# Performance work log

Measured on AMD Instinct MI355X. Metric: run time of the kernel, lower is better.

The kernel has to match this reference:

```python
import jax, jax.numpy as jnp
import numpy as np

# Mamba hyperparams derived from DRMamba.__init__: d_model=dim=96, d_state=16, d_conv=4, expand=2
D_MODEL = 96
D_INNER = 192          # expand * d_model
D_STATE = 16
D_CONV = 4
DT_RANK = 6            # ceil(d_model / 16)
REVERSE = True


def setup_inputs() -> dict:
    key = jax.random.key(0)
    ks = jax.random.split(key, 8)
    s = lambda k, shape: jax.random.normal(k, shape, jnp.float32) * 0.02
    x = jax.random.normal(ks[0], (8, 96, 64, 64), jnp.float32)
    in_proj_w = s(ks[1], (2 * D_INNER, D_MODEL))
    conv_w = s(ks[2], (D_INNER, 1, D_CONV))            # depthwise conv kernel (O, I/groups=1, K)
    conv_b = jnp.zeros((D_INNER,), jnp.float32)
    x_proj_w = s(ks[3], (DT_RANK + 2 * D_STATE, D_INNER))
    dt_proj_w = s(ks[4], (D_INNER, DT_RANK))
    dt_proj_b = s(ks[5], (D_INNER,))
    # S4D-real init, as in standard Mamba
    A_log = jnp.log(jnp.broadcast_to(jnp.arange(1, D_STATE + 1, dtype=jnp.float32), (D_INNER, D_STATE)))
    D = jnp.ones((D_INNER,), jnp.float32)
    out_proj_w = s(ks[6], (D_MODEL, D_INNER))
    return dict(x=x, in_proj_w=in_proj_w, conv_w=conv_w, conv_b=conv_b,
                x_proj_w=x_proj_w, dt_proj_w=dt_proj_w, dt_proj_b=dt_proj_b,
                A_log=A_log, D=D, out_proj_w=out_proj_w)


def reference(x, in_proj_w, conv_w, conv_b, x_proj_w, dt_proj_w, dt_proj_b, A_log, D, out_proj_w):
    b, c, h, w = x.shape
    xs = jnp.flip(x, 1) if REVERSE else x
    seq = xs.reshape(b, c, h * w).transpose(0, 2, 1)              # (b, l, d_model)
    xz = seq @ in_proj_w.T                                        # (b, l, 2*d_inner)
    u, res = jnp.split(xz, 2, axis=-1)
    # causal depthwise conv1d over sequence (torch: padding=d_conv-1 then truncate to l)
    uc = jax.lax.conv_general_dilated(
        u.transpose(0, 2, 1), conv_w, (1,), [(D_CONV - 1, 0)],
        dimension_numbers=('NCH', 'OIH', 'NCH'), feature_group_count=D_INNER)
    uc = uc + conv_b[None, :, None]
    u = jax.nn.silu(uc.transpose(0, 2, 1))                        # (b, l, d_inner)
    # input-dependent SSM parameters
    dbc = u @ x_proj_w.T                                          # (b, l, dt_rank + 2*d_state)
    dt, B, C = jnp.split(dbc, [DT_RANK, DT_RANK + D_STATE], axis=-1)
    delta = jax.nn.softplus(dt @ dt_proj_w.T + dt_proj_b)         # (b, l, d_inner)
    A = -jnp.exp(A_log)                                           # (d_inner, d_state)
    dA = jnp.exp(jnp.einsum('bld,dn->bldn', delta, A))            # discretized A
    dBu = jnp.einsum('bld,bln,bld->bldn', delta, B, u)            # discretized B * u

    def step(state, inp):
        dA_t, dBu_t, C_t = inp                                    # (b,d,n), (b,d,n), (b,n)
        state = dA_t * state + dBu_t
        y_t = jnp.einsum('bdn,bn->bd', state, C_t)
        return state, y_t

    init = jnp.zeros((b, D_INNER, D_STATE), u.dtype)
    _, ys = jax.lax.scan(step, init,
                         (dA.transpose(1, 0, 2, 3), dBu.transpose(1, 0, 2, 3), C.transpose(1, 0, 2)))
    y = ys.transpose(1, 0, 2) + u * D                             # (b, l, d_inner)
    y = y * jax.nn.silu(res)
    out = y @ out_proj_w.T                                        # (b, l, d_model)
    out = out.transpose(0, 2, 1).reshape(b, c, h, w)
    return jnp.flip(out, 1) if REVERSE else out
```

## Files before the change

kernel.cpp:

```cpp
#include <hip/hip_runtime.h>
#include <math.h>

#define NBATCH 8
#define SEQL   4096
#define DMODEL 96
#define DINNER 192
#define DSTATE 16
#define NDBC   38
#define NCHUNK 128
#define CSTEP  32

__device__ __forceinline__ float siluf(float x) {
    return x / (1.f + expf(-x));
}
__device__ __forceinline__ float silu_fast(float x) {
    return x * __builtin_amdgcn_rcpf(1.f + __expf(-x));
}
__device__ __forceinline__ float softplus_fast(float x) {
    return (x > 15.f) ? x : __logf(1.f + __expf(x));
}

__global__ __launch_bounds__(256) void k_in_proj(const float* __restrict__ x,
                                                 const float* __restrict__ w,
                                                 float* __restrict__ u_raw,
                                                 float* __restrict__ res)
{
    __shared__ float As[32][128];
    __shared__ float Wt[32][133];
    const int tid = threadIdx.x;
    const int jg = tid & 15;
    const int lg = tid >> 4;
    const int b = blockIdx.z;
    const int l0 = blockIdx.x * 128;
    const int jb = blockIdx.y * 128;

    float acc[8][8];
#pragma unroll
    for (int r = 0; r < 8; r++)
#pragma unroll
        for (int c = 0; c < 8; c++) acc[r][c] = 0.f;

    for (int kb = 0; kb < 3; kb++) {
        {
            const int ll4 = tid & 31;
            const int m0 = tid >> 5;
#pragma unroll
            for (int i = 0; i < 4; i++) {
                const int m = m0 + 8 * i;
                const float4 v = *reinterpret_cast<const float4*>(
                    &x[((size_t)b * 96 + (95 - (kb * 32 + m))) * 4096 + l0 + ll4 * 4]);
                *reinterpret_cast<float4*>(&As[m][ll4 * 4]) = v;
            }
        }
        {
            const int k4 = tid & 7;
            const int jl0 = tid >> 3;
#pragma unroll
            for (int i = 0; i < 4; i++) {
                const int jl = jl0 + 32 * i;
                const float4 v = *reinterpret_cast<const float4*>(
                    &w[(size_t)(jb + jl) * 96 + kb * 32 + k4 * 4]);
                Wt[k4 * 4 + 0][jl] = v.x;
                Wt[k4 * 4 + 1][jl] = v.y;
                Wt[k4 * 4 + 2][jl] = v.z;
                Wt[k4 * 4 + 3][jl] = v.w;
            }
        }
        __syncthreads();
#pragma unroll
        for (int k = 0; k < 32; k++) {
            const float4 a0 = *reinterpret_cast<const float4*>(&As[k][lg * 8]);
            const float4 a1 = *reinterpret_cast<const float4*>(&As[k][lg * 8 + 4]);
            const float4 w0 = *reinterpret_cast<const float4*>(&Wt[k][jg * 8]);
            const float4 w1 = *reinterpret_cast<const float4*>(&Wt[k][jg * 8 + 4]);
            const float av[8] = {a0.x, a0.y, a0.z, a0.w, a1.x, a1.y, a1.z, a1.w};
            const float wv[8] = {w0.x, w0.y, w0.z, w0.w, w1.x, w1.y, w1.z, w1.w};
#pragma unroll
            for (int r = 0; r < 8; r++)
#pragma unroll
                for (int c = 0; c < 8; c++) acc[r][c] = fmaf(av[r], wv[c], acc[r][c]);
        }
        __syncthreads();
    }

    const int j0 = jb + jg * 8;
    float* outp;
    int col0;
    if (j0 < 192) { outp = u_raw; col0 = j0; }
    else          { outp = res;   col0 = j0 - 192; }
#pragma unroll
    for (int r = 0; r < 8; r++) {
        const int row = l0 + lg * 8 + r;
        float* rowp = &outp[((size_t)b * 4096 + row) * 192 + col0];
        *reinterpret_cast<float4*>(rowp) =
            make_float4(acc[r][0], acc[r][1], acc[r][2], acc[r][3]);
        *reinterpret_cast<float4*>(rowp + 4) =
            make_float4(acc[r][4], acc[r][5], acc[r][6], acc[r][7]);
    }
}

__global__ __launch_bounds__(256) void k_xproj(const float* __restrict__ u_raw,
                                               const float* __restrict__ w,
                                               const float* __restrict__ cw,
                                               const float* __restrict__ cb,
                                               float* __restrict__ dtarr,
                                               float* __restrict__ Barr,
                                               float* __restrict__ Carr)
{
    __shared__ float Ur[67][33];
    __shared__ float Us[64][36];
    __shared__ float Ws[64 * 32];
    const int tid = threadIdx.x, tx = tid & 15, ty = tid >> 4;
    const int b = blockIdx.y;
    const int l0 = blockIdx.x * 64;

    float acc[4][4];
#pragma unroll
    for (int r = 0; r < 4; r++)
#pragma unroll
        for (int c = 0; c < 4; c++) acc[r][c] = 0.f;

    const int ch = tid & 31;
    const int lblk = tid >> 5;

    for (int kb = 0; kb < 6; kb++) {
        for (int idx = tid; idx < 536; idx += 256) {
            const int row = idx >> 3;
            const int c4 = idx & 7;
            const int gl = l0 - 3 + row;
            float4 v = make_float4(0.f, 0.f, 0.f, 0.f);
            if (gl >= 0)
                v = *reinterpret_cast<const float4*>(
                    &u_raw[((size_t)b * 4096 + gl) * 192 + kb * 32 + c4 * 4]);
            Ur[row][c4 * 4 + 0] = v.x;
            Ur[row][c4 * 4 + 1] = v.y;
            Ur[row][c4 * 4 + 2] = v.z;
            Ur[row][c4 * 4 + 3] = v.w;
        }
        {
            const int k4 = tid & 7;
            const int jb0 = tid >> 3;
#pragma unroll
            for (int i = 0; i < 2; i++) {
                const int jl = jb0 + 32 * i;
                float4 v = make_float4(0.f, 0.f, 0.f, 0.f);
                if (jl < NDBC)
                    v = *reinterpret_cast<const float4*>(&w[(size_t)jl * 192 + kb * 32 + k4 * 4]);
                *reinterpret_cast<float4*>(
                    &Ws[jl * 32 + ((k4 ^ ((jl >> 2) & 7)) << 2)]) = v;
            }
        }
        __syncthreads();

        {
            const float4 wc = *reinterpret_cast<const float4*>(&cw[(kb * 32 + ch) * 4]);
            const float bias = cb[kb * 32 + ch];
#pragma unroll
            for (int r = 0; r < 8; r++) {
                const int l = lblk * 8 + r;
                float s = bias;
                s = fmaf(wc.x, Ur[l + 0][ch], s);
                s = fmaf(wc.y, Ur[l + 1][ch], s);
                s = fmaf(wc.z, Ur[l + 2][ch], s);
                s = fmaf(wc.w, Ur[l + 3][ch], s);
                Us[l][ch] = siluf(s);
            }
        }
        __syncthreads();

        const int sw = tx & 7;
#pragma unroll
        for (int k4 = 0; k4 < 8; k4++) {
            float4 a4[4];
#pragma unroll
            for (int r = 0; r < 4; r++)
                a4[r] = *reinterpret_cast<const float4*>(&Us[ty * 4 + r][k4 * 4]);
            float4 w4[4];
#pragma unroll
            for (int c = 0; c < 4; c++)
                w4[c] = *reinterpret_cast<const float4*>(
                    &Ws[(tx * 4 + c) * 32 + ((k4 ^ sw) << 2)]);
#pragma unroll
            for (int r = 0; r < 4; r++)
#pragma unroll
                for (int c = 0; c < 4; c++) {
                    acc[r][c] = fmaf(a4[r].x, w4[c].x, acc[r][c]);
                    acc[r][c] = fmaf(a4[r].y, w4[c].y, acc[r][c]);
                    acc[r][c] = fmaf(a4[r].z, w4[c].z, acc[r][c]);
                    acc[r][c] = fmaf(a4[r].w, w4[c].w, acc[r][c]);
                }
        }
        __syncthreads();
    }

#pragma unroll
    for (int r = 0; r < 4; r++) {
        const size_t row = (size_t)b * 4096 + l0 + ty * 4 + r;
#pragma unroll
        for (int c = 0; c < 4; c++) {
            const int j = tx * 4 + c;
            if (j < 6)       dtarr[row * 8 + j] = acc[r][c];
            else if (j < 22) Barr[row * 16 + (j - 6)] = acc[r][c];
            else if (j < 38) Carr[row * 16 + (j - 22)] = acc[r][c];
        }
    }
}

__global__ __launch_bounds__(192) void k_scan1(const float* __restrict__ u_raw,
                                               const float* __restrict__ dtarr,
                                               const float* __restrict__ Barr,
                                               const float* __restrict__ A_log,
                                               const float* __restrict__ dt_w,
                                               const float* __restrict__ dt_b,
                                               const float* __restrict__ cw,
                                               const float* __restrict__ cb,
                                               float* __restrict__ P,
                                               float* __restrict__ S)
{
    const int d = threadIdx.x;
    const int c = blockIdx.x;
    const int b = blockIdx.y;

    float a[16];
    {
        const float4* al = reinterpret_cast<const float4*>(&A_log[d * 16]);
#pragma unroll
        for (int i = 0; i < 4; i++) {
            const float4 v = al[i];
            a[4 * i + 0] = -expf(v.x);
            a[4 * i + 1] = -expf(v.y);
            a[4 * i + 2] = -expf(v.z);
            a[4 * i + 3] = -expf(v.w);
        }
    }
    float dw[6];
#pragma unroll
    for (int k = 0; k < 6; k++) dw[k] = dt_w[d * 6 + k];
    const float db = dt_b[d];
    const float4 wc = *reinterpret_cast<const float4*>(&cw[d * 4]);
    const float cbias = cb[d];

    float st[16], p[16];
#pragma unroll
    for (int n = 0; n < 16; n++) { st[n] = 0.f; p[n] = 1.f; }

    const int t0 = c * CSTEP;
    const size_t g0 = (size_t)b * 4096 + t0;
    const float* up = u_raw + g0 * 192 + d;
    const float* dtp = dtarr + g0 * 8;
    const float* bp = Barr + g0 * 16;

    float w0 = 0.f, w1 = 0.f, w2 = 0.f;
    if (t0 >= 3) {
        w0 = up[-3 * 192];
        w1 = up[-2 * 192];
        w2 = up[-1 * 192];
    }

#pragma unroll 2
    for (int t = 0; t < CSTEP; t++) {
        const float w3 = up[t * 192];
        float uc = cbias;
        uc = fmaf(wc.x, w0, uc);
        uc = fmaf(wc.y, w1, uc);
        uc = fmaf(wc.z, w2, uc);
        uc = fmaf(wc.w, w3, uc);
        w0 = w1; w1 = w2; w2 = w3;
        const float ut = silu_fast(uc);

        const float4 q0 = *reinterpret_cast<const float4*>(dtp + t * 8);
        const float4 q1 = *reinterpret_cast<const float4*>(dtp + t * 8 + 4);
        float s = db;
        s = fmaf(q0.x, dw[0], s); s = fmaf(q0.y, dw[1], s);
        s = fmaf(q0.z, dw[2], s); s = fmaf(q0.w, dw[3], s);
        s = fmaf(q1.x, dw[4], s); s = fmaf(q1.y, dw[5], s);
        const float dt = softplus_fast(s);
        const float dtu = dt * ut;

        float Bv[16];
        {
            const float4* b4 = reinterpret_cast<const float4*>(bp + t * 16);
#pragma unroll
            for (int i = 0; i < 4; i++) {
                const float4 v = b4[i];
                Bv[4 * i + 0] = v.x; Bv[4 * i + 1] = v.y;
                Bv[4 * i + 2] = v.z; Bv[4 * i + 3] = v.w;
            }
        }
#pragma unroll
        for (int n = 0; n < 16; n++) {
            const float dA = __expf(dt * a[n]);
            p[n] *= dA;
            st[n] = fmaf(dA, st[n], dtu * Bv[n]);
        }
    }

    const size_t idx = (((size_t)b * NCHUNK + c) * 192 + d) * 16;
    float4* Pp = reinterpret_cast<float4*>(&P[idx]);
    float4* Sp = reinterpret_cast<float4*>(&S[idx]);
#pragma unroll
    for (int i = 0; i < 4; i++) {
        Pp[i] = make_float4(p[4 * i], p[4 * i + 1], p[4 * i + 2], p[4 * i + 3]);
        Sp[i] = make_float4(st[4 * i], st[4 * i + 1], st[4 * i + 2], st[4 * i + 3]);
    }
}

__global__ __launch_bounds__(256) void k_scan2(const float* __restrict__ P,
                                               float* __restrict__ S)
{
    const int dn = blockIdx.x * 256 + threadIdx.x;
    const int b = blockIdx.y;
    float carry = 0.f;
    const size_t base = (size_t)b * NCHUNK * 3072 + dn;
#pragma unroll 8
    for (int c = 0; c < NCHUNK; c++) {
        const size_t idx = base + (size_t)c * 3072;
        const float p = P[idx];
        const float s = S[idx];
        S[idx] = carry;
        carry = fmaf(p, carry, s);
    }
}

__global__ __launch_bounds__(192) void k_scan3(const float* __restrict__ u_raw,
                                               const float* __restrict__ dtarr,
                                               const float* __restrict__ Barr,
                                               const float* __restrict__ Carr,
                                               const float* __restrict__ A_log,
                                               const float* __restrict__ dt_w,
                                               const float* __restrict__ dt_b,
                                               const float* __restrict__ cw,
                                               const float* __restrict__ cb,
                                               const float* __restrict__ S,
                                               const float* __restrict__ Dp,
                                               const float* __restrict__ res,
                                               float* __restrict__ y)
{
    const int d = threadIdx.x;
    const int c = blockIdx.x;
    const int b = blockIdx.y;

    float a[16];
    {
        const float4* al = reinterpret_cast<const float4*>(&A_log[d * 16]);
#pragma unroll
        for (int i = 0; i < 4; i++) {
            const float4 v = al[i];
            a[4 * i + 0] = -expf(v.x);
            a[4 * i + 1] = -expf(v.y);
            a[4 * i + 2] = -expf(v.z);
            a[4 * i + 3] = -expf(v.w);
        }
    }
    float dw[6];
#pragma unroll
    for (int k = 0; k < 6; k++) dw[k] = dt_w[d * 6 + k];
    const float db = dt_b[d];
    const float4 wc = *reinterpret_cast<const float4*>(&cw[d * 4]);
    const float cbias = cb[d];
    const float Dd = Dp[d];

    float st[16];
    {
        const float4* Sp = reinterpret_cast<const float4*>(
            &S[(((size_t)b * NCHUNK + c) * 192 + d) * 16]);
#pragma unroll
        for (int i = 0; i < 4; i++) {
            const float4 v = Sp[i];
            st[4 * i + 0] = v.x; st[4 * i + 1] = v.y;
            st[4 * i + 2] = v.z; st[4 * i + 3] = v.w;
        }
    }

    const int t0 = c * CSTEP;
    const size_t g0 = (size_t)b * 4096 + t0;
    const float* up = u_raw + g0 * 192 + d;
    const float* rp = res + g0 * 192 + d;
    float* yp = y + g0 * 192 + d;
    const float* dtp = dtarr + g0 * 8;
    const float* bp = Barr + g0 * 16;
    const float* cp = Carr + g0 * 16;

    float w0 = 0.f, w1 = 0.f, w2 = 0.f;
    if (t0 >= 3) {
        w0 = up[-3 * 192];
        w1 = up[-2 * 192];
        w2 = up[-1 * 192];
    }

#pragma unroll 2
    for (int t = 0; t < CSTEP; t++) {
        const float w3 = up[t * 192];
        float uc = cbias;
        uc = fmaf(wc.x, w0, uc);
        uc = fmaf(wc.y, w1, uc);
        uc = fmaf(wc.z, w2, uc);
        uc = fmaf(wc.w, w3, uc);
        w0 = w1; w1 = w2; w2 = w3;
        const float ut = silu_fast(uc);

        const float4 q0 = *reinterpret_cast<const float4*>(dtp + t * 8);
        const float4 q1 = *reinterpret_cast<const float4*>(dtp + t * 8 + 4);
        float s = db;
        s = fmaf(q0.x, dw[0], s); s = fmaf(q0.y, dw[1], s);
        s = fmaf(q0.z, dw[2], s); s = fmaf(q0.w, dw[3], s);
        s = fmaf(q1.x, dw[4], s); s = fmaf(q1.y, dw[5], s);
        const float dt = softplus_fast(s);
        const float dtu = dt * ut;

        float Bv[16], Cv[16];
        {
            const float4* b4 = reinterpret_cast<const float4*>(bp + t * 16);
            const float4* c4 = reinterpret_cast<const float4*>(cp + t * 16);
#pragma unroll
            for (int i = 0; i < 4; i++) {
                const float4 v = b4[i];
                Bv[4 * i + 0] = v.x; Bv[4 * i + 1] = v.y;
                Bv[4 * i + 2] = v.z; Bv[4 * i + 3] = v.w;
                const float4 w = c4[i];
                Cv[4 * i + 0] = w.x; Cv[4 * i + 1] = w.y;
                Cv[4 * i + 2] = w.z; Cv[4 * i + 3] = w.w;
            }
        }
        float yt = 0.f;
#pragma unroll
        for (int n = 0; n < 16; n++) {
            const float dA = __expf(dt * a[n]);
            st[n] = fmaf(dA, st[n], dtu * Bv[n]);
            yt = fmaf(st[n], Cv[n], yt);
        }
        const float r = rp[t * 192];
        yp[t * 192] = fmaf(ut, Dd, yt) * silu_fast(r);
    }
}

__global__ __launch_bounds__(256) void k_outproj(const float* __restrict__ y,
                                                 const float* __restrict__ w,
                                                 float* __restrict__ out)
{
    __shared__ float Ws[64 * 32];
    const int tid = threadIdx.x, tx = tid & 15, ty = tid >> 4;
    const int b = blockIdx.z;
    const int l0 = blockIdx.x * 128;
    const int jb = blockIdx.y * 64;

    float acc[8][4];
#pragma unroll
    for (int r = 0; r < 8; r++)
#pragma unroll
        for (int c = 0; c < 4; c++) acc[r][c] = 0.f;

    for (int kb = 0; kb < 6; kb++) {
        {
            const int k4 = tid & 7;
            const int jb0 = tid >> 3;
#pragma unroll
            for (int i = 0; i < 2; i++) {
                const int jl = jb0 + 32 * i;
                const int j = jb + jl;
                float4 v = make_float4(0.f, 0.f, 0.f, 0.f);
                if (j < 96)
                    v = *reinterpret_cast<const float4*>(&w[(size_t)j * 192 + kb * 32 + k4 * 4]);
                *reinterpret_cast<float4*>(
                    &Ws[jl * 32 + ((k4 ^ ((jl >> 2) & 7)) << 2)]) = v;
            }
        }
        __syncthreads();
        const int sw = tx & 7;
#pragma unroll
        for (int k4 = 0; k4 < 8; k4++) {
            float4 a4[8];
#pragma unroll
            for (int r = 0; r < 8; r++) {
                const int row = l0 + ty * 8 + r;
                a4[r] = *reinterpret_cast<const float4*>(
                    &y[((size_t)b * 4096 + row) * 192 + kb * 32 + k4 * 4]);
            }
            float4 w4[4];
#pragma unroll
            for (int c = 0; c < 4; c++)
                w4[c] = *reinterpret_cast<const float4*>(
                    &Ws[(tx * 4 + c) * 32 + ((k4 ^ sw) << 2)]);
#pragma unroll
            for (int r = 0; r < 8; r++)
#pragma unroll
                for (int c = 0; c < 4; c++) {
                    acc[r][c] = fmaf(a4[r].x, w4[c].x, acc[r][c]);
                    acc[r][c] = fmaf(a4[r].y, w4[c].y, acc[r][c]);
                    acc[r][c] = fmaf(a4[r].z, w4[c].z, acc[r][c]);
                    acc[r][c] = fmaf(a4[r].w, w4[c].w, acc[r][c]);
                }
        }
        __syncthreads();
    }
#pragma unroll
    for (int c = 0; c < 4; c++) {
        const int j = jb + tx * 4 + c;
        if (j < 96) {
            const int ch = 95 - j;
            const float4 v0 = make_float4(acc[0][c], acc[1][c], acc[2][c], acc[3][c]);
            const float4 v1 = make_float4(acc[4][c], acc[5][c], acc[6][c], acc[7][c]);
            const size_t base = ((size_t)b * 96 + ch) * 4096 + l0 + ty * 8;
            *reinterpret_cast<float4*>(&out[base]) = v0;
            *reinterpret_cast<float4*>(&out[base + 4]) = v1;
        }
    }
}

extern "C" void kernel_launch(void* const* d_in, const int* in_sizes, int n_in,
                              void* d_out, int out_size, void* d_ws, size_t ws_size,
                              hipStream_t stream)
{
    const float* x       = (const float*)d_in[0];
    const float* in_w    = (const float*)d_in[1];
    const float* conv_w  = (const float*)d_in[2];
    const float* conv_b  = (const float*)d_in[3];
    const float* xproj_w = (const float*)d_in[4];
    const float* dt_w    = (const float*)d_in[5];
    const float* dt_b    = (const float*)d_in[6];
    const float* A_log   = (const float*)d_in[7];
    const float* Dp      = (const float*)d_in[8];
    const float* out_w   = (const float*)d_in[9];

    float* ws    = (float*)d_ws;
    float* u_raw = ws;
    float* res   = u_raw + 6291456;
    float* yfin  = res   + 6291456;
    float* dtarr = yfin  + 6291456;
    float* Barr  = dtarr + 262144;
    float* Carr  = Barr  + 524288;
    float* P     = Carr  + 524288;
    float* S     = P     + 3145728;

    hipLaunchKernelGGL(k_in_proj, dim3(32, 3, 8), dim3(256), 0, stream, x, in_w, u_raw, res);
    hipLaunchKernelGGL(k_xproj,   dim3(64, 8),    dim3(256), 0, stream,
                       u_raw, xproj_w, conv_w, conv_b, dtarr, Barr, Carr);
    hipLaunchKernelGGL(k_scan1,   dim3(NCHUNK, 8), dim3(192), 0, stream,
                       u_raw, dtarr, Barr, A_log, dt_w, dt_b, conv_w, conv_b, P, S);
    hipLaunchKernelGGL(k_scan2,   dim3(12, 8),    dim3(256), 0, stream, P, S);
    hipLaunchKernelGGL(k_scan3,   dim3(NCHUNK, 8), dim3(192), 0, stream,
                       u_raw, dtarr, Barr, Carr, A_log, dt_w, dt_b, conv_w, conv_b,
                       S, Dp, res, yfin);
    hipLaunchKernelGGL(k_outproj, dim3(32, 2, 8), dim3(256), 0, stream, yfin, out_w, (float*)d_out);
}
```

Measured before the change: 274.0 us.

## Retile in_proj GEMM with 512-thread blocks, 256-row by 64-column tiles

Restructures the input projection GEMM. Each block now covers 256 sequence positions by 64 output columns with 512 threads, and each thread computes 4 rows by 8 columns, where before it was 128x128 tiles, 256 threads and 8x8 per thread. Within a wave, every lane reads its own A values while all lanes read the same W values as a broadcast. The goal is to cut LDS bank conflicts, lower register pressure for better occupancy, and raise the block count. In exchange, each thread does less arithmetic per LDS load, and each block reloads the x tile for every 64-column slice, which increases global reads of x.

```diff
diff --git a/kernel.cpp b/kernel.cpp
--- a/kernel.cpp
+++ b/kernel.cpp
@@ -20,77 +20,70 @@
     return (x > 15.f) ? x : __logf(1.f + __expf(x));
 }
 
-__global__ __launch_bounds__(256) void k_in_proj(const float* __restrict__ x,
+__global__ __launch_bounds__(512) void k_in_proj(const float* __restrict__ x,
                                                  const float* __restrict__ w,
                                                  float* __restrict__ u_raw,
                                                  float* __restrict__ res)
 {
-    __shared__ float As[32][128];
-    __shared__ float Wt[32][133];
+    __shared__ float As[32][256];
+    __shared__ float Wt[32][72];
     const int tid = threadIdx.x;
-    const int jg = tid & 15;
-    const int lg = tid >> 4;
+    const int lane = tid & 63;
+    const int wv = tid >> 6;
     const int b = blockIdx.z;
-    const int l0 = blockIdx.x * 128;
-    const int jb = blockIdx.y * 128;
-
-    float acc[8][8];
-#pragma unroll
-    for (int r = 0; r < 8; r++)
+    const int l0 = blockIdx.y * 256;
+    const int jb = blockIdx.x * 64;
+    const int j0 = jb + wv * 8;
+
+    float acc[4][8];
+#pragma unroll
+    for (int r = 0; r < 4; r++)
 #pragma unroll
         for (int c = 0; c < 8; c++) acc[r][c] = 0.f;
 
     for (int kb = 0; kb < 3; kb++) {
+#pragma unroll
+        for (int i = 0; i < 4; i++) {
+            const int idx = tid + 512 * i;
+            const int m = idx >> 6;
+            const int c4 = idx & 63;
+            const float4 v = *reinterpret_cast<const float4*>(
+                &x[((size_t)b * 96 + (95 - (kb * 32 + m))) * 4096 + l0 + c4 * 4]);
+            *reinterpret_cast<float4*>(&As[m][c4 * 4]) = v;
+        }
         {
-            const int ll4 = tid & 31;
-            const int m0 = tid >> 5;
-#pragma unroll
-            for (int i = 0; i < 4; i++) {
-                const int m = m0 + 8 * i;
-                const float4 v = *reinterpret_cast<const float4*>(
-                    &x[((size_t)b * 96 + (95 - (kb * 32 + m))) * 4096 + l0 + ll4 * 4]);
-                *reinterpret_cast<float4*>(&As[m][ll4 * 4]) = v;
-            }
-        }
-        {
-            const int k4 = tid & 7;
-            const int jl0 = tid >> 3;
-#pragma unroll
-            for (int i = 0; i < 4; i++) {
-                const int jl = jl0 + 32 * i;
-                const float4 v = *reinterpret_cast<const float4*>(
-                    &w[(size_t)(jb + jl) * 96 + kb * 32 + k4 * 4]);
-                Wt[k4 * 4 + 0][jl] = v.x;
-                Wt[k4 * 4 + 1][jl] = v.y;
-                Wt[k4 * 4 + 2][jl] = v.z;
-                Wt[k4 * 4 + 3][jl] = v.w;
-            }
+            const int j = tid & 63;
+            const int k4 = tid >> 6;
+            const float4 v = *reinterpret_cast<const float4*>(
+                &w[(size_t)(jb + j) * 96 + kb * 32 + k4 * 4]);
+            Wt[k4 * 4 + 0][j] = v.x;
+            Wt[k4 * 4 + 1][j] = v.y;
+            Wt[k4 * 4 + 2][j] = v.z;
+            Wt[k4 * 4 + 3][j] = v.w;
         }
         __syncthreads();
 #pragma unroll
         for (int k = 0; k < 32; k++) {
-            const float4 a0 = *reinterpret_cast<const float4*>(&As[k][lg * 8]);
-            const float4 a1 = *reinterpret_cast<const float4*>(&As[k][lg * 8 + 4]);
-            const float4 w0 = *reinterpret_cast<const float4*>(&Wt[k][jg * 8]);
-            const float4 w1 = *reinterpret_cast<const float4*>(&Wt[k][jg * 8 + 4]);
-            const float av[8] = {a0.x, a0.y, a0.z, a0.w, a1.x, a1.y, a1.z, a1.w};
-            const float wv[8] = {w0.x, w0.y, w0.z, w0.w, w1.x, w1.y, w1.z, w1.w};
-#pragma unroll
-            for (int r = 0; r < 8; r++)
-#pragma unroll
-                for (int c = 0; c < 8; c++) acc[r][c] = fmaf(av[r], wv[c], acc[r][c]);
-        }
-        __syncthreads();
-    }
-
-    const int j0 = jb + jg * 8;
+            const float4 a4 = *reinterpret_cast<const float4*>(&As[k][lane * 4]);
+            const float4 wA = *reinterpret_cast<const float4*>(&Wt[k][wv * 8]);
+            const float4 wB = *reinterpret_cast<const float4*>(&Wt[k][wv * 8 + 4]);
+            const float av[4] = {a4.x, a4.y, a4.z, a4.w};
+            const float wvv[8] = {wA.x, wA.y, wA.z, wA.w, wB.x, wB.y, wB.z, wB.w};
+#pragma unroll
+            for (int r = 0; r < 4; r++)
+#pragma unroll
+                for (int c = 0; c < 8; c++) acc[r][c] = fmaf(av[r], wvv[c], acc[r][c]);
+        }
+        __syncthreads();
+    }
+
     float* outp;
     int col0;
     if (j0 < 192) { outp = u_raw; col0 = j0; }
     else          { outp = res;   col0 = j0 - 192; }
 #pragma unroll
-    for (int r = 0; r < 8; r++) {
-        const int row = l0 + lg * 8 + r;
+    for (int r = 0; r < 4; r++) {
+        const int row = l0 + lane * 4 + r;
         float* rowp = &outp[((size_t)b * 4096 + row) * 192 + col0];
         *reinterpret_cast<float4*>(rowp) =
             make_float4(acc[r][0], acc[r][1], acc[r][2], acc[r][3]);
@@ -532,7 +525,7 @@
     float* P     = Carr  + 524288;
     float* S     = P     + 3145728;
 
-    hipLaunchKernelGGL(k_in_proj, dim3(32, 3, 8), dim3(256), 0, stream, x, in_w, u_raw, res);
+    hipLaunchKernelGGL(k_in_proj, dim3(6, 16, 8), dim3(512), 0, stream, x, in_w, u_raw, res);
     hipLaunchKernelGGL(k_xproj,   dim3(64, 8),    dim3(256), 0, stream,
                        u_raw, xproj_w, conv_w, conv_b, dtarr, Barr, Carr);
     hipLaunchKernelGGL(k_scan1,   dim3(NCHUNK, 8), dim3(192), 0, stream,
```

Measured after the change: 273.2 us. No clear change (-0.3%).
